# Performance work log

Measured on AMD Instinct MI355X. Metric: run time of the kernel, lower is better.

Reference implementation:

```python
import jax, jax.numpy as jnp
import numpy as np

B, Nq, C, H = 1, 300, 256, 8
h, w = 32, 32
HW = h * w
HID = 512  # rpe_hidden_dim
HD = C // H


def setup_inputs() -> dict:
    key = jax.random.key(0)
    ks = jax.random.split(key, 16)
    s = 0.02
    inp = {
        "raw_query": jax.random.normal(ks[0], (B, Nq, C), jnp.float32),
        "query_pos": jax.random.normal(ks[1], (B, Nq, C), jnp.float32),
        "reference_points": jax.random.uniform(ks[2], (B, Nq, 2), jnp.float32),
        "raw_src": jax.random.normal(ks[3], (B, HW, C), jnp.float32),
        "src_pos_embed": jax.random.normal(ks[4], (B, HW, C), jnp.float32),
        "Wq": jax.random.normal(ks[5], (C, C), jnp.float32) * s,
        "bq": jnp.zeros((C,), jnp.float32),
        "Wk": jax.random.normal(ks[6], (C, C), jnp.float32) * s,
        "bk": jnp.zeros((C,), jnp.float32),
        "Wv": jax.random.normal(ks[7], (C, C), jnp.float32) * s,
        "bv": jnp.zeros((C,), jnp.float32),
        "Wo": jax.random.normal(ks[8], (C, C), jnp.float32) * s,
        "bo": jnp.zeros((C,), jnp.float32),
        "W1": jax.random.normal(ks[9], (HID, 2), jnp.float32),   # cpb MLP layer 1
        "b1": jnp.zeros((HID,), jnp.float32),
        "W2": jax.random.normal(ks[10], (H, HID), jnp.float32) * s,  # cpb MLP layer 2 (no bias)
        "input_spatial_shapes": np.array([[h, w]], dtype=np.int64),
    }
    return inp


def _key_positions(hh, ww):
    ys = (jnp.arange(hh, dtype=jnp.float32) + 0.5) / hh
    xs = (jnp.arange(ww, dtype=jnp.float32) + 0.5) / ww
    yy, xx = jnp.meshgrid(ys, xs, indexing="ij")  # row-major: idx = y*w + x
    return jnp.stack([xx.ravel(), yy.ravel()], axis=-1)  # [HW, 2] (x, y)


def reference(raw_query, query_pos, reference_points, raw_src, src_pos_embed,
              Wq, bq, Wk, bk, Wv, bv, Wo, bo, W1, b1, W2, input_spatial_shapes):
    hh, ww = int(input_spatial_shapes[0, 0]), int(input_spatial_shapes[0, 1])
    scale = HD ** (-0.5)
    queries = raw_query + query_pos                      # [B,Nq,C]
    memory = raw_src + src_pos_embed                     # [B,HW,C]

    q = (queries @ Wq.T + bq).reshape(B, Nq, H, HD)
    k = (memory @ Wk.T + bk).reshape(B, hh * ww, H, HD)
    v = (memory @ Wv.T + bv).reshape(B, hh * ww, H, HD)

    logits = jnp.einsum("bqhd,bkhd->bhqk", q, k) * scale  # [B,H,Nq,HW]

    key_pos = _key_positions(hh, ww)                      # [HW,2]
    delta = reference_points[:, :, None, :] - key_pos[None, None]  # [B,Nq,HW,2]
    hid = jax.nn.relu(jnp.einsum("bqkc,hc->bqkh", delta, W1) + b1)  # [B,Nq,HW,HID]
    bias = jnp.einsum("bqkf,hf->bhqk", hid, W2)           # [B,H,Nq,HW]

    attn = jax.nn.softmax(logits + bias, axis=-1)
    out = jnp.einsum("bhqk,bkhd->bqhd", attn, v).reshape(B, Nq, C)
    return out @ Wo.T + bo
```

## Files before the change

kernel.cpp:

```cpp
#include <hip/hip_runtime.h>
#include <hip/hip_fp16.h>
#include <stdint.h>

#define NQ   300
#define CDIM 256
#define NH   8
#define HD   32
#define HWK  1024
#define HIDD 512

typedef __attribute__((ext_vector_type(8))) _Float16 f16x8;
typedef __attribute__((ext_vector_type(2))) _Float16 h2v;
typedef __attribute__((ext_vector_type(4))) float f32x4;

#define QB_OFF   0
#define KB_OFF   153600
#define VT_OFF   677888
#define PO_OFF   1202176
#define PL_OFF   3659776
#define A16_OFF  3736576
#define NX_OFF   4043776
#define NY_OFF   4044800
#define W2_OFF   4045824

__device__ __forceinline__ short f16b(float x){
  _Float16 h = (_Float16)x;
  return __builtin_bit_cast(short, h);
}

__device__ __forceinline__ uint32_t pk_f16(float a, float b){
  auto r = __builtin_amdgcn_cvt_pkrtz(a, b);
  return __builtin_bit_cast(uint32_t, r);
}

__device__ __forceinline__ h2v cvt2h(float a, float b){
  auto r = __builtin_amdgcn_cvt_pkrtz(a, b);
  return __builtin_bit_cast(h2v, r);
}

__global__ __launch_bounds__(256) void prep_kernel(
    const float* __restrict__ refp, const float* __restrict__ W1,
    const float* __restrict__ b1, const float* __restrict__ W2,
    short* __restrict__ a16, short* __restrict__ nx16,
    short* __restrict__ ny16, short* __restrict__ w216)
{
  int idx = blockIdx.x * 256 + threadIdx.x;
  if (idx < NQ*HIDD){
    int q = idx >> 9, f = idx & 511;
    float2 w = ((const float2*)W1)[f];
    float a = fmaf(w.x, refp[2*q], fmaf(w.y, refp[2*q+1], b1[f]));
    a16[idx] = f16b(a);
  } else {
    int j = idx - NQ*HIDD;
    if (j < HIDD){
      float2 w = ((const float2*)W1)[j];
      nx16[j] = f16b(-w.x);
      ny16[j] = f16b(-w.y);
    } else if (j < HIDD + NH*HIDD){
      int e = j - HIDD;
      w216[e] = f16b(W2[e]);
    }
  }
}

__global__ __launch_bounds__(256) void proj_kernel(
    const float* __restrict__ rq, const float* __restrict__ qp,
    const float* __restrict__ rs, const float* __restrict__ spe,
    const float* __restrict__ Wq, const float* __restrict__ bq,
    const float* __restrict__ Wk, const float* __restrict__ bk,
    const float* __restrict__ Wv, const float* __restrict__ bv,
    const float* __restrict__ Wo, const float* __restrict__ bo,
    char* __restrict__ ws, float* __restrict__ dout, int final_mode)
{
  int bxid = blockIdx.x;
  int tile = bxid >> 1, half = bxid & 1;
  const float *in1, *in2, *W, *bias;
  int r0, M, mode;
  const float* po = (const float*)(ws + PO_OFF);
  const float* pl = (const float*)(ws + PL_OFF);
  if (final_mode){
    in1 = po; in2 = nullptr; W = Wo; bias = bo;
    r0 = tile*16; M = NQ; mode = 3;
  } else if (tile < 19){
    in1 = rq; in2 = qp; W = Wq; bias = bq; r0 = tile*16; M = NQ; mode = 0;
  } else if (tile < 83){
    in1 = rs; in2 = spe; W = Wk; bias = bk; r0 = (tile-19)*16; M = HWK; mode = 1;
  } else {
    in1 = rs; in2 = spe; W = Wv; bias = bv; r0 = (tile-83)*16; M = HWK; mode = 2;
  }
  __shared__ __align__(16) float At[32][20];
  __shared__ float Wl[32][129];
  __shared__ float linv[16][8];
  int tid = threadIdx.x;
  int n_loc = tid & 127;
  int rg = tid >> 7;
  int n = half*128 + n_loc;
  float acc[8];
  float bv_ = bias[n];
  #pragma unroll
  for (int i=0;i<8;i++) acc[i] = bv_;

  if (mode == 3 && tid < 128){
    int r = tid >> 3, hh = tid & 7;
    int gr = r0 + r; if (gr >= M) gr = M - 1;
    float s = 0.f;
    #pragma unroll
    for (int p = 0; p < 8; p++) s += pl[((size_t)p*NQ+gr)*NH+hh];
    linv[r][hh] = 1.0f / s;
  }

  for (int c0 = 0; c0 < CDIM; c0 += 32){
    __syncthreads();
    for (int e = tid; e < 512; e += 256){
      int r = e >> 5, c = e & 31;
      int gr = r0 + r; if (gr >= M) gr = M - 1;
      float v;
      if (mode == 3){
        int cc = c0 + c;
        v = 0.f;
        #pragma unroll
        for (int p = 0; p < 8; p++) v += po[(size_t)(p*NQ+gr)*CDIM + cc];
        v *= linv[r][c0 >> 5];
      } else {
        v = in1[gr*CDIM + c0 + c];
        if (in2) v += in2[gr*CDIM + c0 + c];
      }
      At[c][r] = v;
    }
    for (int e = tid; e < 4096; e += 256){
      int c = e & 31, nn = e >> 5;
      Wl[c][nn] = W[(half*128 + nn)*CDIM + c0 + c];
    }
    __syncthreads();
    #pragma unroll
    for (int c = 0; c < 32; c++){
      float w = Wl[c][n_loc];
      const float4* ap = (const float4*)&At[c][rg*8];
      float4 a0 = ap[0], a1 = ap[1];
      acc[0] = fmaf(a0.x, w, acc[0]);
      acc[1] = fmaf(a0.y, w, acc[1]);
      acc[2] = fmaf(a0.z, w, acc[2]);
      acc[3] = fmaf(a0.w, w, acc[3]);
      acc[4] = fmaf(a1.x, w, acc[4]);
      acc[5] = fmaf(a1.y, w, acc[5]);
      acc[6] = fmaf(a1.z, w, acc[6]);
      acc[7] = fmaf(a1.w, w, acc[7]);
    }
  }

  if (mode == 0){
    short* qb = (short*)(ws + QB_OFF);
    const float s = 0.17677669529663687f;
    #pragma unroll
    for (int i=0;i<8;i++){
      int gr = r0 + rg*8 + i;
      if (gr < M) qb[gr*CDIM + n] = f16b(acc[i]*s);
    }
  } else if (mode == 1){
    short* kb = (short*)(ws + KB_OFF);
    int h = n >> 5, d = n & 31;
    #pragma unroll
    for (int i=0;i<8;i++){
      int gr = r0 + rg*8 + i;
      if (gr < M) kb[((size_t)h*HWK + gr)*HD + d] = f16b(acc[i]);
    }
  } else if (mode == 2){
    short* vt = (short*)(ws + VT_OFF);
    uint32_t p[4];
    #pragma unroll
    for (int i=0;i<4;i++) p[i] = pk_f16(acc[2*i], acc[2*i+1]);
    *(uint4*)(vt + n*HWK + r0 + rg*8) = make_uint4(p[0], p[1], p[2], p[3]);
  } else {
    #pragma unroll
    for (int i=0;i<8;i++){
      int gr = r0 + rg*8 + i;
      if (gr < M) dout[gr*CDIM + n] = acc[i];
    }
  }
}

__global__ __launch_bounds__(256, 4) void fused_kernel(
    const short* __restrict__ a16, const short* __restrict__ nx16,
    const short* __restrict__ ny16, const short* __restrict__ w216,
    const short* __restrict__ qb, const short* __restrict__ kb,
    const short* __restrict__ vt, float* __restrict__ po,
    float* __restrict__ pl)
{
  int bid = blockIdx.x;
  int q0 = (bid >> 3) * 2, kr = bid & 7;
  int tid = threadIdx.x, wave = tid >> 6, lane = tid & 63;
  int n = lane & 15, qd = lane >> 4;

  __shared__ __align__(16) _Float16 nwx[HIDD];
  __shared__ __align__(16) char pool[8192];
  __shared__ __align__(16) _Float16 w2l[NH][520];
  __shared__ __align__(16) _Float16 pb[2][NH][136];
  __shared__ float lsum[4][16];
  _Float16 (*c1s)[4][HIDD] = (_Float16 (*)[4][HIDD])pool;
  float (*part)[4][NH][32] = (float (*)[4][NH][32])pool;

  {
    int f0 = tid * 2;
    h2v ny2 = *(const h2v*)(ny16 + f0);
    h2v nx2 = *(const h2v*)(nx16 + f0);
    *(h2v*)&nwx[f0] = nx2;
    #pragma unroll
    for (int qq = 0; qq < 2; qq++){
      h2v a2 = *(const h2v*)(a16 + (q0+qq)*HIDD + f0);
      #pragma unroll
      for (int r = 0; r < 4; r++){
        _Float16 kyh = (_Float16)(((float)(kr*4 + r) + 0.5f) * (1.0f/32.0f));
        h2v ky2 = {kyh, kyh};
        *(h2v*)&c1s[qq][r][f0] = ny2 * ky2 + a2;
      }
    }
  }
  for (int e = tid; e < 512; e += 256){
    int r = e >> 6, c = e & 63;
    *(f16x8*)&w2l[r][c*8] = *(const f16x8*)(w216 + r*HIDD + c*8);
  }
  f16x8 qfrag = *(const f16x8*)(qb + (q0 + (n >> 3))*CDIM + (n & 7)*HD + qd*8);
  f16x8 qm[NH];
  #pragma unroll
  for (int h = 0; h < NH; h++){
    f16x8 z = {0,0,0,0,0,0,0,0};
    qm[h] = ((n & 7) == h) ? qfrag : z;
  }
  __syncthreads();

  const int kyrow = kr*4 + wave;
  const int kbase = kyrow * 32;

  f32x4 acc1[2] = {{0.f,0.f,0.f,0.f},{0.f,0.f,0.f,0.f}};
  #pragma unroll
  for (int t = 0; t < 2; t++){
    int k0 = kbase + t*16;
    #pragma unroll
    for (int h = 0; h < NH; h++){
      f16x8 af = *(const f16x8*)(kb + ((size_t)h*HWK + k0 + n)*HD + qd*8);
      acc1[t] = __builtin_amdgcn_mfma_f32_16x16x32_f16(af, qm[h], acc1[t], 0, 0, 0);
    }
  }

  _Float16 kxAh = (_Float16)(((float)n + 0.5f) * (1.0f/32.0f));
  _Float16 kxBh = (_Float16)(((float)n + 16.5f) * (1.0f/32.0f));
  f16x8 kxA8, kxB8, z8;
  #pragma unroll
  for (int j = 0; j < 8; j++){ kxA8[j] = kxAh; kxB8[j] = kxBh; z8[j] = (_Float16)0.f; }
  f32x4 accb[2][2];
  accb[0][0] = acc1[0]; accb[0][1] = acc1[1];
  accb[1][0] = acc1[0]; accb[1][1] = acc1[1];
  const _Float16* c1r0 = &c1s[0][wave][0];
  const _Float16* c1r1 = &c1s[1][wave][0];
  #pragma unroll 4
  for (int kc = 0; kc < 16; kc++){
    int f0 = kc*32 + qd*8;
    f16x8 c10 = *(const f16x8*)(c1r0 + f0);
    f16x8 c11 = *(const f16x8*)(c1r1 + f0);
    f16x8 wxv = *(const f16x8*)(&nwx[f0]);
    f16x8 bfr = *(const f16x8*)(&w2l[n & 7][f0]);
    #pragma unroll
    for (int t = 0; t < 2; t++){
      f16x8 kx8 = t ? kxB8 : kxA8;
      f16x8 e0 = __builtin_elementwise_max(wxv * kx8 + c10, z8);
      accb[0][t] = __builtin_amdgcn_mfma_f32_16x16x32_f16(e0, bfr, accb[0][t], 0, 0, 0);
      f16x8 e1 = __builtin_elementwise_max(wxv * kx8 + c11, z8);
      accb[1][t] = __builtin_amdgcn_mfma_f32_16x16x32_f16(e1, bfr, accb[1][t], 0, 0, 0);
    }
  }

  int qsel = n >> 3, hsel = n & 7;
  float lacc = 0.f;
  #pragma unroll
  for (int t = 0; t < 2; t++){
    f32x4 a = qsel ? accb[1][t] : accb[0][t];
    float e0 = __expf(a[0]);
    float e1 = __expf(a[1]);
    float e2 = __expf(a[2]);
    float e3 = __expf(a[3]);
    uint2 p2;
    p2.x = pk_f16(e0, e1);
    p2.y = pk_f16(e2, e3);
    *(uint2*)&pb[qsel][hsel][wave*32 + t*16 + qd*4] = p2;
    float s = e0 + e1 + e2 + e3;
    s += __shfl_xor(s, 16);
    s += __shfl_xor(s, 32);
    lacc += s;
  }
  if (lane < 16) lsum[wave][lane] = lacc;

  #pragma unroll
  for (int h = 0; h < NH; h++){
    int kl = wave*32 + qd*8;
    f16x8 pa = *(const f16x8*)&pb[n & 1][h][kl];
    f16x8 v0 = *(const f16x8*)(vt + ((size_t)(h*HD +      n))*HWK + kr*128 + kl);
    f16x8 v1 = *(const f16x8*)(vt + ((size_t)(h*HD + 16 + n))*HWK + kr*128 + kl);
    f32x4 o0 = {0.f,0.f,0.f,0.f}, o1 = {0.f,0.f,0.f,0.f};
    o0 = __builtin_amdgcn_mfma_f32_16x16x32_f16(pa, v0, o0, 0, 0, 0);
    o1 = __builtin_amdgcn_mfma_f32_16x16x32_f16(pa, v1, o1, 0, 0, 0);
    if (qd == 0){
      part[0][wave][h][n]      = o0[0];
      part[1][wave][h][n]      = o0[1];
      part[0][wave][h][16 + n] = o1[0];
      part[1][wave][h][16 + n] = o1[1];
    }
  }
  __syncthreads();

  {
    int h = tid >> 5, d = tid & 31;
    #pragma unroll
    for (int qq = 0; qq < 2; qq++){
      float s = part[qq][0][h][d] + part[qq][1][h][d]
              + part[qq][2][h][d] + part[qq][3][h][d];
      po[((size_t)kr*NQ + q0 + qq)*CDIM + tid] = s;
    }
    if (tid < 16){
      float s = lsum[0][tid] + lsum[1][tid] + lsum[2][tid] + lsum[3][tid];
      pl[((size_t)kr*NQ + q0 + (tid >> 3))*NH + (tid & 7)] = s;
    }
  }
}

extern "C" void kernel_launch(void* const* d_in, const int* in_sizes, int n_in,
                              void* d_out, int out_size, void* d_ws, size_t ws_size,
                              hipStream_t stream)
{
  const float* rq  = (const float*)d_in[0];
  const float* qp  = (const float*)d_in[1];
  const float* rp  = (const float*)d_in[2];
  const float* rs  = (const float*)d_in[3];
  const float* spe = (const float*)d_in[4];
  const float* Wq  = (const float*)d_in[5];
  const float* bq  = (const float*)d_in[6];
  const float* Wk  = (const float*)d_in[7];
  const float* bk  = (const float*)d_in[8];
  const float* Wv  = (const float*)d_in[9];
  const float* bv  = (const float*)d_in[10];
  const float* Wo  = (const float*)d_in[11];
  const float* bo  = (const float*)d_in[12];
  const float* W1  = (const float*)d_in[13];
  const float* b1  = (const float*)d_in[14];
  const float* W2  = (const float*)d_in[15];
  char* ws = (char*)d_ws;
  float* dout = (float*)d_out;

  prep_kernel<<<618, 256, 0, stream>>>(rp, W1, b1, W2,
      (short*)(ws + A16_OFF), (short*)(ws + NX_OFF),
      (short*)(ws + NY_OFF), (short*)(ws + W2_OFF));
  proj_kernel<<<294, 256, 0, stream>>>(rq, qp, rs, spe, Wq, bq, Wk, bk,
      Wv, bv, Wo, bo, ws, dout, 0);
  fused_kernel<<<1200, 256, 0, stream>>>((const short*)(ws + A16_OFF),
      (const short*)(ws + NX_OFF), (const short*)(ws + NY_OFF),
      (const short*)(ws + W2_OFF), (const short*)(ws + QB_OFF),
      (const short*)(ws + KB_OFF), (const short*)(ws + VT_OFF),
      (float*)(ws + PO_OFF), (float*)(ws + PL_OFF));
  proj_kernel<<<38, 256, 0, stream>>>(rq, qp, rs, spe, Wq, bq, Wk, bk,
      Wv, bv, Wo, bo, ws, dout, 1);
}
```

Baseline: 155.5 us.

## Merge prep into projection launch and add dedicated per-query output projection kernel

Folds the prep work (fp16 hidden pre-activations, negated W1 columns, W2 conversion) into extra blocks of the Q/K/V projection launch, removing one kernel launch and letting the two independent jobs share the grid. Replaces the final Wo projection mode of proj_kernel with a separate kernel that uses one block per query. That kernel reduces the 8 partial outputs and the softmax denominators, then computes the 256 outputs with one thread per output row reading Wo rows directly. This raises final-stage parallelism from 38 to 300 blocks, but each thread now streams a full Wo row with strided, uncoalesced access.

```diff
diff --git a/kernel.cpp b/kernel.cpp
--- a/kernel.cpp
+++ b/kernel.cpp
@@ -33,64 +33,55 @@
   return __builtin_bit_cast(uint32_t, r);
 }
 
-__device__ __forceinline__ h2v cvt2h(float a, float b){
-  auto r = __builtin_amdgcn_cvt_pkrtz(a, b);
-  return __builtin_bit_cast(h2v, r);
-}
-
-__global__ __launch_bounds__(256) void prep_kernel(
-    const float* __restrict__ refp, const float* __restrict__ W1,
-    const float* __restrict__ b1, const float* __restrict__ W2,
-    short* __restrict__ a16, short* __restrict__ nx16,
-    short* __restrict__ ny16, short* __restrict__ w216)
-{
-  int idx = blockIdx.x * 256 + threadIdx.x;
-  if (idx < NQ*HIDD){
-    int q = idx >> 9, f = idx & 511;
-    float2 w = ((const float2*)W1)[f];
-    float a = fmaf(w.x, refp[2*q], fmaf(w.y, refp[2*q+1], b1[f]));
-    a16[idx] = f16b(a);
-  } else {
-    int j = idx - NQ*HIDD;
-    if (j < HIDD){
-      float2 w = ((const float2*)W1)[j];
-      nx16[j] = f16b(-w.x);
-      ny16[j] = f16b(-w.y);
-    } else if (j < HIDD + NH*HIDD){
-      int e = j - HIDD;
-      w216[e] = f16b(W2[e]);
-    }
-  }
-}
-
 __global__ __launch_bounds__(256) void proj_kernel(
     const float* __restrict__ rq, const float* __restrict__ qp,
     const float* __restrict__ rs, const float* __restrict__ spe,
     const float* __restrict__ Wq, const float* __restrict__ bq,
     const float* __restrict__ Wk, const float* __restrict__ bk,
     const float* __restrict__ Wv, const float* __restrict__ bv,
-    const float* __restrict__ Wo, const float* __restrict__ bo,
-    char* __restrict__ ws, float* __restrict__ dout, int final_mode)
+    const float* __restrict__ refp, const float* __restrict__ W1,
+    const float* __restrict__ b1, const float* __restrict__ W2,
+    char* __restrict__ ws)
 {
   int bxid = blockIdx.x;
+  __shared__ __align__(16) float At[32][20];
+  __shared__ float Wl[32][129];
+
+  if (bxid >= 294){
+    int idx = (bxid - 294) * 256 + threadIdx.x;
+    short* a16  = (short*)(ws + A16_OFF);
+    short* nx16 = (short*)(ws + NX_OFF);
+    short* ny16 = (short*)(ws + NY_OFF);
+    short* w216 = (short*)(ws + W2_OFF);
+    if (idx < NQ*HIDD){
+      int q = idx >> 9, f = idx & 511;
+      float2 w = ((const float2*)W1)[f];
+      float a = fmaf(w.x, refp[2*q], fmaf(w.y, refp[2*q+1], b1[f]));
+      a16[idx] = f16b(a);
+    } else {
+      int j = idx - NQ*HIDD;
+      if (j < HIDD){
+        float2 w = ((const float2*)W1)[j];
+        nx16[j] = f16b(-w.x);
+        ny16[j] = f16b(-w.y);
+      } else if (j < HIDD + NH*HIDD){
+        int e = j - HIDD;
+        w216[e] = f16b(W2[e]);
+      }
+    }
+    return;
+  }
+
   int tile = bxid >> 1, half = bxid & 1;
   const float *in1, *in2, *W, *bias;
   int r0, M, mode;
-  const float* po = (const float*)(ws + PO_OFF);
-  const float* pl = (const float*)(ws + PL_OFF);
-  if (final_mode){
-    in1 = po; in2 = nullptr; W = Wo; bias = bo;
-    r0 = tile*16; M = NQ; mode = 3;
-  } else if (tile < 19){
+  if (tile < 19){
     in1 = rq; in2 = qp; W = Wq; bias = bq; r0 = tile*16; M = NQ; mode = 0;
   } else if (tile < 83){
     in1 = rs; in2 = spe; W = Wk; bias = bk; r0 = (tile-19)*16; M = HWK; mode = 1;
   } else {
     in1 = rs; in2 = spe; W = Wv; bias = bv; r0 = (tile-83)*16; M = HWK; mode = 2;
   }
-  __shared__ __align__(16) float At[32][20];
-  __shared__ float Wl[32][129];
-  __shared__ float linv[16][8];
   int tid = threadIdx.x;
   int n_loc = tid & 127;
   int rg = tid >> 7;
@@ -100,32 +91,12 @@
   #pragma unroll
   for (int i=0;i<8;i++) acc[i] = bv_;
 
-  if (mode == 3 && tid < 128){
-    int r = tid >> 3, hh = tid & 7;
-    int gr = r0 + r; if (gr >= M) gr = M - 1;
-    float s = 0.f;
-    #pragma unroll
-    for (int p = 0; p < 8; p++) s += pl[((size_t)p*NQ+gr)*NH+hh];
-    linv[r][hh] = 1.0f / s;
-  }
-
   for (int c0 = 0; c0 < CDIM; c0 += 32){
     __syncthreads();
     for (int e = tid; e < 512; e += 256){
       int r = e >> 5, c = e & 31;
       int gr = r0 + r; if (gr >= M) gr = M - 1;
-      float v;
-      if (mode == 3){
-        int cc = c0 + c;
-        v = 0.f;
-        #pragma unroll
-        for (int p = 0; p < 8; p++) v += po[(size_t)(p*NQ+gr)*CDIM + cc];
-        v *= linv[r][c0 >> 5];
-      } else {
-        v = in1[gr*CDIM + c0 + c];
-        if (in2) v += in2[gr*CDIM + c0 + c];
-      }
-      At[c][r] = v;
+      At[c][r] = in1[gr*CDIM + c0 + c] + in2[gr*CDIM + c0 + c];
     }
     for (int e = tid; e < 4096; e += 256){
       int c = e & 31, nn = e >> 5;
@@ -164,18 +135,12 @@
       int gr = r0 + rg*8 + i;
       if (gr < M) kb[((size_t)h*HWK + gr)*HD + d] = f16b(acc[i]);
     }
-  } else if (mode == 2){
+  } else {
     short* vt = (short*)(ws + VT_OFF);
     uint32_t p[4];
     #pragma unroll
     for (int i=0;i<4;i++) p[i] = pk_f16(acc[2*i], acc[2*i+1]);
     *(uint4*)(vt + n*HWK + r0 + rg*8) = make_uint4(p[0], p[1], p[2], p[3]);
-  } else {
-    #pragma unroll
-    for (int i=0;i<8;i++){
-      int gr = r0 + rg*8 + i;
-      if (gr < M) dout[gr*CDIM + n] = acc[i];
-    }
   }
 }
 
@@ -320,6 +285,49 @@
       pl[((size_t)kr*NQ + q0 + (tid >> 3))*NH + (tid & 7)] = s;
     }
   }
+}
+
+__global__ __launch_bounds__(256) void outproj_kernel(
+    const float* __restrict__ po, const float* __restrict__ pl,
+    const float* __restrict__ Wo, const float* __restrict__ bo,
+    float* __restrict__ dout)
+{
+  int q = blockIdx.x;
+  int tid = threadIdx.x;
+  __shared__ __align__(16) float a_lds[CDIM];
+  __shared__ float linv[NH];
+
+  float s = 0.f;
+  #pragma unroll
+  for (int p = 0; p < 8; p++) s += po[((size_t)p*NQ + q)*CDIM + tid];
+
+  if (tid < 64){
+    int p = tid >> 3, h = tid & 7;
+    float l = pl[((size_t)p*NQ + q)*NH + h];
+    l += __shfl_xor(l, 8);
+    l += __shfl_xor(l, 16);
+    l += __shfl_xor(l, 32);
+    if (p == 0) linv[h] = 1.0f / l;
+  }
+  __syncthreads();
+  a_lds[tid] = s * linv[tid >> 5];
+  __syncthreads();
+
+  const float4* wrow = (const float4*)(Wo + (size_t)tid*CDIM);
+  const float4* av = (const float4*)a_lds;
+  float acc0 = bo[tid], acc1 = 0.f, acc2 = 0.f, acc3 = 0.f;
+  #pragma unroll 4
+  for (int c = 0; c < 64; c += 4){
+    float4 w0 = wrow[c+0], a0 = av[c+0];
+    float4 w1 = wrow[c+1], a1 = av[c+1];
+    float4 w2 = wrow[c+2], a2 = av[c+2];
+    float4 w3 = wrow[c+3], a3 = av[c+3];
+    acc0 = fmaf(w0.x,a0.x,fmaf(w0.y,a0.y,fmaf(w0.z,a0.z,fmaf(w0.w,a0.w,acc0))));
+    acc1 = fmaf(w1.x,a1.x,fmaf(w1.y,a1.y,fmaf(w1.z,a1.z,fmaf(w1.w,a1.w,acc1))));
+    acc2 = fmaf(w2.x,a2.x,fmaf(w2.y,a2.y,fmaf(w2.z,a2.z,fmaf(w2.w,a2.w,acc2))));
+    acc3 = fmaf(w3.x,a3.x,fmaf(w3.y,a3.y,fmaf(w3.z,a3.z,fmaf(w3.w,a3.w,acc3))));
+  }
+  dout[(size_t)q*CDIM + tid] = acc0 + acc1 + acc2 + acc3;
 }
 
 extern "C" void kernel_launch(void* const* d_in, const int* in_sizes, int n_in,
@@ -345,16 +353,13 @@
   char* ws = (char*)d_ws;
   float* dout = (float*)d_out;
 
-  prep_kernel<<<618, 256, 0, stream>>>(rp, W1, b1, W2,
-      (short*)(ws + A16_OFF), (short*)(ws + NX_OFF),
-      (short*)(ws + NY_OFF), (short*)(ws + W2_OFF));
-  proj_kernel<<<294, 256, 0, stream>>>(rq, qp, rs, spe, Wq, bq, Wk, bk,
-      Wv, bv, Wo, bo, ws, dout, 0);
+  proj_kernel<<<912, 256, 0, stream>>>(rq, qp, rs, spe, Wq, bq, Wk, bk,
+      Wv, bv, rp, W1, b1, W2, ws);
   fused_kernel<<<1200, 256, 0, stream>>>((const short*)(ws + A16_OFF),
       (const short*)(ws + NX_OFF), (const short*)(ws + NY_OFF),
       (const short*)(ws + W2_OFF), (const short*)(ws + QB_OFF),
       (const short*)(ws + KB_OFF), (const short*)(ws + VT_OFF),
       (float*)(ws + PO_OFF), (float*)(ws + PL_OFF));
-  proj_kernel<<<38, 256, 0, stream>>>(rq, qp, rs, spe, Wq, bq, Wk, bk,
-      Wv, bv, Wo, bo, ws, dout, 1);
-}
+  outproj_kernel<<<300, 256, 0, stream>>>((const float*)(ws + PO_OFF),
+      (const float*)(ws + PL_OFF), Wo, bo, dout);
+}
```

New measurement: 144.3 us. 7.2% less time.
